# Kernel tuning notes

Measured on AMD Instinct MI355X. Metric: run time of the kernel, lower is better.

Reference implementation:

```python
import jax, jax.numpy as jnp
import numpy as np

N, E, G = 100000, 800000, 64
F_IN, H = 92, 4
D1, D2, D3 = 32, 64, 128  # per-head out dims: hidden//2, hidden, 2*hidden
HID, LAT = 64, 128
FINAL = H * D3  # 512
NEG_SLOPE = 0.2


def _p(key, shape, scale=0.05):
    return jax.random.normal(key, shape, dtype=jnp.float32) * scale


def setup_inputs() -> dict:
    key = jax.random.key(0)
    ks = jax.random.split(key, 32)
    node_feat = jax.random.normal(ks[0], (N, F_IN), dtype=jnp.float32)
    src = jax.random.randint(ks[1], (E,), 0, N)
    dst = jax.random.randint(ks[2], (E,), 0, N)
    graph_id = jnp.sort(jax.random.randint(ks[3], (N,), 0, G))
    d = {"node_feat": node_feat, "src": src, "dst": dst, "graph_id": graph_id}
    # GAT layer params (DGL GATConv: fc no bias, attn_l/attn_r [H,D], bias [H*D])
    dims = [(F_IN, D1), (H * D1, D2), (H * D2, D3)]
    i = 4
    for li, (fi, do) in enumerate(dims, 1):
        d[f"W{li}"] = _p(ks[i], (fi, H * do)); i += 1
        d[f"al{li}"] = _p(ks[i], (H, do)); i += 1
        d[f"ar{li}"] = _p(ks[i], (H, do)); i += 1
        d[f"b{li}"] = jnp.zeros((H * do,), dtype=jnp.float32)
    # gate MLP: Linear(final, hid) -> ReLU -> Linear(hid, 1)
    d["Wg1"] = _p(ks[i], (FINAL, HID)); i += 1
    d["bg1"] = jnp.zeros((HID,), dtype=jnp.float32)
    d["Wg2"] = _p(ks[i], (HID, 1)); i += 1
    d["bg2"] = jnp.zeros((1,), dtype=jnp.float32)
    d["Wmu"] = _p(ks[i], (FINAL, LAT)); i += 1
    d["bmu"] = jnp.zeros((LAT,), dtype=jnp.float32)
    d["Wlv"] = _p(ks[i], (FINAL, LAT)); i += 1
    d["blv"] = jnp.zeros((LAT,), dtype=jnp.float32)
    return d


def gat_layer(h, W, al, ar, b, src, dst, heads, d_out):
    n = h.shape[0]
    Wh = (h @ W).reshape(n, heads, d_out)                      # [N,H,D]
    el = jnp.einsum('nhd,hd->nh', Wh, al)                      # a_l . Wh
    er = jnp.einsum('nhd,hd->nh', Wh, ar)
    e = jax.nn.leaky_relu(el[src] + er[dst], NEG_SLOPE)        # [E,H]
    m = jax.ops.segment_max(e, dst, num_segments=n)
    m = jnp.where(jnp.isfinite(m), m, 0.0)                     # zero-in-degree guard
    ex = jnp.exp(e - m[dst])
    s = jax.ops.segment_sum(ex, dst, num_segments=n)
    a = ex / jnp.maximum(s[dst], 1e-9)                         # edge softmax
    msg = a[:, :, None] * Wh[src]                              # [E,H,D] (peak intermediate)
    out = jax.ops.segment_sum(msg, dst, num_segments=n)        # scatter-aggregate
    out = out + b.reshape(1, heads, d_out)
    return out.reshape(n, heads * d_out)                       # flatten(1)


def attention_pool(h, graph_id, Wg1, bg1, Wg2, bg2, num_graphs):
    gate = jax.nn.relu(h @ Wg1 + bg1) @ Wg2 + bg2              # [N,1]
    m = jax.ops.segment_max(gate, graph_id, num_segments=num_graphs)
    ex = jnp.exp(gate - m[graph_id])
    s = jax.ops.segment_sum(ex, graph_id, num_segments=num_graphs)
    a = ex / jnp.maximum(s[graph_id], 1e-9)                    # softmax over nodes per graph
    return jax.ops.segment_sum(a * h, graph_id, num_segments=num_graphs)  # [G,final]


def reference(node_feat, src, dst, graph_id,
              W1, al1, ar1, b1, W2, al2, ar2, b2, W3, al3, ar3, b3,
              Wg1, bg1, Wg2, bg2, Wmu, bmu, Wlv, blv):
    h = jax.nn.elu(gat_layer(node_feat, W1, al1, ar1, b1, src, dst, H, D1))
    h = jax.nn.elu(gat_layer(h, W2, al2, ar2, b2, src, dst, H, D2))
    h = jax.nn.elu(gat_layer(h, W3, al3, ar3, b3, src, dst, H, D3))
    g = attention_pool(h, graph_id, Wg1, bg1, Wg2, bg2, G)
    mu = g @ Wmu + bmu
    logvar = g @ Wlv + blv
    return (mu, logvar)
```

## Files before the change

kernel.cpp:

```cpp
#include <hip/hip_runtime.h>
#include <math.h>

#define NNODES 100000
#define NEDGES 800000
#define NGRAPH 64
#define NHEAD  4
#define FINALD 512
#define HIDG   64
#define LATD   128
#define K1P    96
#define NB_SCAN 98
#define PQ     16

typedef unsigned int uint;
typedef unsigned short ushort;
typedef __attribute__((ext_vector_type(8))) short bf16x8;
typedef __attribute__((ext_vector_type(4))) float f32x4;

__device__ __forceinline__ float bflo(uint u) { return __uint_as_float(u << 16); }
__device__ __forceinline__ float bfhi(uint u) { return __uint_as_float(u & 0xffff0000u); }
__device__ __forceinline__ ushort f2bf(float f) {
    uint u = __float_as_uint(f);
    return (ushort)((u + 0x7fffu + ((u >> 16) & 1u)) >> 16);
}
__device__ __forceinline__ uint pack2(float a, float b) {
    return (uint)f2bf(a) | ((uint)f2bf(b) << 16);
}
__device__ __forceinline__ void fmabf2(float w, uint v, float& a0, float& a1) {
    a0 = fmaf(w, bflo(v), a0);
    a1 = fmaf(w, bfhi(v), a1);
}

__device__ __forceinline__ void async_copy16(const ushort* gsrc, ushort* lds_base) {
    __builtin_amdgcn_global_load_lds(
        (const __attribute__((address_space(1))) uint*)gsrc,
        (__attribute__((address_space(3))) uint*)lds_base,
        16, 0, 0);
}

__global__ void init_kernel(int* __restrict__ deg, const int* __restrict__ gid,
                            int* __restrict__ gstart) {
    int i = blockIdx.x * blockDim.x + threadIdx.x;
    if (i < NNODES) deg[i] = 0;
    if (i <= NGRAPH) {
        int lo = 0, hi = NNODES;
        while (lo < hi) {
            int mid = (lo + hi) >> 1;
            if (gid[mid] < i) lo = mid + 1; else hi = mid;
        }
        gstart[i] = lo;
    }
}
__global__ void count_kernel(const int* __restrict__ dst, int* __restrict__ deg) {
    int e = blockIdx.x * blockDim.x + threadIdx.x;
    if (e < NEDGES) atomicAdd(&deg[dst[e]], 1);
}
__global__ __launch_bounds__(1024) void scan_block_kernel(const int* __restrict__ deg,
                                                          int* __restrict__ off,
                                                          int* __restrict__ bsum) {
    __shared__ int buf[1024];
    int t = threadIdx.x;
    int i = blockIdx.x * 1024 + t;
    int x = (i < NNODES) ? deg[i] : 0;
    buf[t] = x;
    __syncthreads();
    for (int s = 1; s < 1024; s <<= 1) {
        int v = (t >= s) ? buf[t - s] : 0;
        __syncthreads();
        buf[t] += v;
        __syncthreads();
    }
    if (i < NNODES) off[i] = buf[t] - x;
    if (t == 1023) bsum[blockIdx.x] = buf[1023];
}
__global__ __launch_bounds__(128) void scan_bsum_kernel(int* __restrict__ bsum) {
    __shared__ int buf[128];
    int t = threadIdx.x;
    int x = (t < NB_SCAN) ? bsum[t] : 0;
    buf[t] = x;
    __syncthreads();
    for (int s = 1; s < 128; s <<= 1) {
        int v = (t >= s) ? buf[t - s] : 0;
        __syncthreads();
        buf[t] += v;
        __syncthreads();
    }
    if (t < NB_SCAN) bsum[t] = buf[t] - x;
    if (t == 0) bsum[NB_SCAN] = buf[NB_SCAN - 1];
}
__global__ __launch_bounds__(1024) void scan_add_kernel(int* __restrict__ off,
                                                        const int* __restrict__ bsum,
                                                        int* __restrict__ cursor) {
    int i = blockIdx.x * 1024 + threadIdx.x;
    if (i < NNODES) {
        int v = off[i] + bsum[blockIdx.x];
        off[i] = v;
        cursor[i] = v;
    }
    if (i == 0) off[NNODES] = bsum[NB_SCAN];
}
__global__ void scatter_kernel(const int* __restrict__ src, const int* __restrict__ dst,
                               int* __restrict__ cursor, int* __restrict__ src_csr) {
    int e = blockIdx.x * blockDim.x + threadIdx.x;
    if (e >= NEDGES) return;
    int p = atomicAdd(&cursor[dst[e]], 1);
    src_csr[p] = src[e];
}

#define C1 (128 * K1P)
#define C2 (256 * 128)
#define C3 (512 * 256)
#define CG (64 * 512)
#define CX (NNODES * K1P)
#define CTOT (C1 + C2 + C3 + CG + CX + NNODES)
__global__ void conv_all_kernel(const float* __restrict__ W1, const float* __restrict__ W2,
                                const float* __restrict__ W3, const float* __restrict__ Wg1,
                                const float* __restrict__ nf,
                                ushort* __restrict__ Bt1, ushort* __restrict__ Bt2,
                                ushort* __restrict__ Bt3, ushort* __restrict__ Btg,
                                ushort* __restrict__ x0, float* __restrict__ gate) {
    int i = blockIdx.x * blockDim.x + threadIdx.x;
    if (i < C1) {
        int n = i / K1P, k = i - n * K1P;
        Bt1[i] = (k < 92) ? f2bf(W1[(size_t)k * 128 + n]) : (ushort)0;
        return;
    }
    i -= C1;
    if (i < C2) {
        int n = i >> 7, k = i & 127;
        Bt2[i] = f2bf(W2[(size_t)k * 256 + n]);
        return;
    }
    i -= C2;
    if (i < C3) {
        int n = i >> 8, k = i & 255;
        Bt3[i] = f2bf(W3[(size_t)k * 512 + n]);
        return;
    }
    i -= C3;
    if (i < CG) {
        int n = i >> 9, k = i & 511;
        Btg[i] = f2bf(Wg1[(size_t)k * 64 + n]);
        return;
    }
    i -= CG;
    if (i < CX) {
        int n = i / K1P, k = i - n * K1P;
        x0[i] = (k < 92) ? f2bf(nf[(size_t)n * 92 + k]) : (ushort)0;
        return;
    }
    i -= CX;
    if (i < NNODES) gate[i] = 0.f;
}

template <int BN, int MODE>
__global__ __launch_bounds__(256) void mfma_gemm(const ushort* __restrict__ A,
                                                 const ushort* __restrict__ Bt,
                                                 const float* __restrict__ bias,
                                                 ushort* __restrict__ C,
                                                 const float* __restrict__ Wg2,
                                                 float* __restrict__ gate,
                                                 int M, int K, int N) {
    constexpr int WNS = BN / 2;
    constexpr int NT = WNS / 16;
    __shared__ ushort Alds[128][32];
    __shared__ ushort Blds[BN][32];
    int tid = threadIdx.x;
    int wave = tid >> 6, lane = tid & 63;
    int wm = wave & 1, wn = wave >> 1;
    int quad = lane >> 4, l16 = lane & 15;
    int rowBase = blockIdx.y * 128;
    int colBase = blockIdx.x * BN;

    int srow = lane >> 2;
    int scol = (lane & 3) * 8;

    f32x4 acc[4][NT];
#pragma unroll
    for (int i = 0; i < 4; i++)
#pragma unroll
        for (int j = 0; j < NT; j++) acc[i][j] = (f32x4){0.f, 0.f, 0.f, 0.f};

    for (int k0 = 0; k0 < K; k0 += 32) {
#pragma unroll
        for (int c = 0; c < 2; c++) {
            int chunk = wave * 2 + c;
            int row = rowBase + chunk * 16 + srow;
            async_copy16(&A[(size_t)row * K + k0 + scol], &Alds[chunk * 16][0]);
        }
        if constexpr (BN == 128) {
#pragma unroll
            for (int c = 0; c < 2; c++) {
                int chunk = wave * 2 + c;
                int row = colBase + chunk * 16 + srow;
                async_copy16(&Bt[(size_t)row * K + k0 + scol], &Blds[chunk * 16][0]);
            }
        } else {
            int row = colBase + wave * 16 + srow;
            async_copy16(&Bt[(size_t)row * K + k0 + scol], &Blds[wave * 16][0]);
        }
        __syncthreads();
        bf16x8 af[4], bf[NT];
#pragma unroll
        for (int i = 0; i < 4; i++)
            af[i] = *(const bf16x8*)&Alds[wm * 64 + i * 16 + l16][quad * 8];
#pragma unroll
        for (int j = 0; j < NT; j++)
            bf[j] = *(const bf16x8*)&Blds[wn * WNS + j * 16 + l16][quad * 8];
#pragma unroll
        for (int i = 0; i < 4; i++)
#pragma unroll
            for (int j = 0; j < NT; j++)
                acc[i][j] = __builtin_amdgcn_mfma_f32_16x16x32_bf16(af[i], bf[j], acc[i][j], 0, 0, 0);
        __syncthreads();
    }

    if constexpr (MODE == 0) {
#pragma unroll
        for (int i = 0; i < 4; i++) {
#pragma unroll
            for (int j = 0; j < NT; j++) {
                int col = colBase + wn * WNS + j * 16 + l16;
#pragma unroll
                for (int r = 0; r < 4; r++) {
                    int row = rowBase + wm * 64 + i * 16 + quad * 4 + r;
                    if (row < M) C[(size_t)row * N + col] = f2bf(acc[i][j][r]);
                }
            }
        }
    } else {
        float bb[NT], wg[NT];
#pragma unroll
        for (int j = 0; j < NT; j++) {
            int col = colBase + wn * WNS + j * 16 + l16;
            bb[j] = bias[col];
            wg[j] = Wg2[col];
        }
#pragma unroll
        for (int i = 0; i < 4; i++) {
            float pd[4] = {0.f, 0.f, 0.f, 0.f};
#pragma unroll
            for (int j = 0; j < NT; j++) {
#pragma unroll
                for (int r = 0; r < 4; r++) {
                    float x = fmaxf(acc[i][j][r] + bb[j], 0.f);
                    pd[r] = fmaf(x, wg[j], pd[r]);
                }
            }
#pragma unroll
            for (int m = 1; m < 16; m <<= 1)
#pragma unroll
                for (int r = 0; r < 4; r++)
                    pd[r] += __shfl_xor(pd[r], m, 64);
            if (l16 == 0) {
#pragma unroll
                for (int r = 0; r < 4; r++) {
                    int row = rowBase + wm * 64 + i * 16 + quad * 4 + r;
                    if (row < M) atomicAdd(&gate[row], pd[r]);
                }
            }
        }
    }
}

template <int HD>
__global__ __launch_bounds__(256) void eler_node(const ushort* __restrict__ Wh,
                                                 const float* __restrict__ al,
                                                 const float* __restrict__ ar,
                                                 float* __restrict__ el,
                                                 float* __restrict__ er) {
    constexpr int LPN = HD / 8;
    constexpr int NPW = 64 / LPN;
    constexpr int S = (HD / NHEAD) / 8;
    int wave = threadIdx.x >> 6;
    int lane = threadIdx.x & 63;
    int sub = lane & (LPN - 1);
    int n = blockIdx.x * (4 * NPW) + wave * NPW + lane / LPN;
    int d0 = sub * 8;
    uint4 v = *(const uint4*)&Wh[(size_t)n * HD + d0];
    float w0 = bflo(v.x), w1 = bfhi(v.x), w2 = bflo(v.y), w3 = bfhi(v.y);
    float w4 = bflo(v.z), w5 = bfhi(v.z), w6 = bflo(v.w), w7 = bfhi(v.w);
    float4 a0 = *(const float4*)&al[d0];
    float4 a1 = *(const float4*)&al[d0 + 4];
    float4 b0 = *(const float4*)&ar[d0];
    float4 b1 = *(const float4*)&ar[d0 + 4];
    float sl, sr;
    sl = w0 * a0.x; sl = fmaf(w1, a0.y, sl); sl = fmaf(w2, a0.z, sl); sl = fmaf(w3, a0.w, sl);
    sl = fmaf(w4, a1.x, sl); sl = fmaf(w5, a1.y, sl); sl = fmaf(w6, a1.z, sl); sl = fmaf(w7, a1.w, sl);
    sr = w0 * b0.x; sr = fmaf(w1, b0.y, sr); sr = fmaf(w2, b0.z, sr); sr = fmaf(w3, b0.w, sr);
    sr = fmaf(w4, b1.x, sr); sr = fmaf(w5, b1.y, sr); sr = fmaf(w6, b1.z, sr); sr = fmaf(w7, b1.w, sr);
#pragma unroll
    for (int o = S / 2; o > 0; o >>= 1) {
        sl += __shfl_down(sl, o, 64);
        sr += __shfl_down(sr, o, 64);
    }
    if ((sub & (S - 1)) == 0) {
        int h = sub / S;
        el[n * 4 + h] = sl;
        er[n * 4 + h] = sr;
    }
}

__global__ void attn_node(const int* __restrict__ src_csr, const int* __restrict__ off,
                          const float4* __restrict__ el4, const float4* __restrict__ er4,
                          float4* __restrict__ aw4, float4* __restrict__ m4) {
    int n = blockIdx.x * blockDim.x + threadIdx.x;
    if (n >= NNODES) return;
    int i0 = off[n], i1 = off[n + 1];
    float4 ern = er4[n];
    float m0 = -1e30f, m1 = -1e30f, m2 = -1e30f, m3 = -1e30f;
    for (int i = i0; i < i1; i += 8) {
        int cnt = i1 - i; if (cnt > 8) cnt = 8;
        int s8[8];
#pragma unroll
        for (int j = 0; j < 8; j++)
            if (j < cnt) s8[j] = src_csr[i + j];
        float4 e8[8];
#pragma unroll
        for (int j = 0; j < 8; j++)
            if (j < cnt) e8[j] = el4[s8[j]];
#pragma unroll
        for (int j = 0; j < 8; j++) {
            if (j < cnt) {
                float4 x = e8[j];
                x.x += ern.x; x.y += ern.y; x.z += ern.z; x.w += ern.w;
                x.x = (x.x >= 0.f) ? x.x : 0.2f * x.x;
                x.y = (x.y >= 0.f) ? x.y : 0.2f * x.y;
                x.z = (x.z >= 0.f) ? x.z : 0.2f * x.z;
                x.w = (x.w >= 0.f) ? x.w : 0.2f * x.w;
                aw4[i + j] = x;
                m0 = fmaxf(m0, x.x); m1 = fmaxf(m1, x.y);
                m2 = fmaxf(m2, x.z); m3 = fmaxf(m3, x.w);
            }
        }
    }
    m4[n] = make_float4(m0, m1, m2, m3);
}

template <int HD, int DPL, int B>
__global__ __launch_bounds__(256) void gat_aggregate4(const int* __restrict__ src_csr,
                                                      const int* __restrict__ off,
                                                      const ushort* __restrict__ Wh,
                                                      const float* __restrict__ aw,
                                                      const float* __restrict__ m4,
                                                      const float* __restrict__ bias,
                                                      ushort* __restrict__ out,
                                                      int pass) {
    constexpr int LOGD = (HD == 128) ? 5 : (HD == 256) ? 6 : 7;
    const int lane = threadIdx.x & 63;
    const int wv = __builtin_amdgcn_readfirstlane((int)(threadIdx.x >> 6));
    const int n = blockIdx.x * 4 + wv;
    const int d = pass * (64 * DPL) + lane * DPL;
    const int h = d >> LOGD;
    const int i0 = __builtin_amdgcn_readfirstlane(off[n]);
    const int i1 = __builtin_amdgcn_readfirstlane(off[n + 1]);
    const float mh = m4[n * 4 + h];

    float acc[DPL];
#pragma unroll
    for (int j = 0; j < DPL; j++) acc[j] = 0.f;
    float ssum = 0.f;
    const ushort* __restrict__ col = Wh + d;

    int i = i0;
    for (; i + B <= i1; i += B) {
        int s[B];
        float w[B];
#pragma unroll
        for (int b = 0; b < B; b++) s[b] = __builtin_amdgcn_readfirstlane(src_csr[i + b]);
#pragma unroll
        for (int b = 0; b < B; b++) w[b] = expf(aw[(size_t)(i + b) * 4 + h] - mh);
        if constexpr (DPL == 8) {
            uint4 v[B];
#pragma unroll
            for (int b = 0; b < B; b++) v[b] = *(const uint4*)&col[(size_t)s[b] * HD];
#pragma unroll
            for (int b = 0; b < B; b++) {
                ssum += w[b];
                fmabf2(w[b], v[b].x, acc[0], acc[1]);
                fmabf2(w[b], v[b].y, acc[2], acc[3]);
                fmabf2(w[b], v[b].z, acc[4], acc[5]);
                fmabf2(w[b], v[b].w, acc[6], acc[7]);
            }
        } else if constexpr (DPL == 4) {
            uint2 v[B];
#pragma unroll
            for (int b = 0; b < B; b++) v[b] = *(const uint2*)&col[(size_t)s[b] * HD];
#pragma unroll
            for (int b = 0; b < B; b++) {
                ssum += w[b];
                fmabf2(w[b], v[b].x, acc[0], acc[1]);
                fmabf2(w[b], v[b].y, acc[2], acc[3]);
            }
        } else {
            uint v[B];
#pragma unroll
            for (int b = 0; b < B; b++) v[b] = *(const uint*)&col[(size_t)s[b] * HD];
#pragma unroll
            for (int b = 0; b < B; b++) {
                ssum += w[b];
                fmabf2(w[b], v[b], acc[0], acc[1]);
            }
        }
    }
    for (; i < i1; ++i) {
        const int s0 = __builtin_amdgcn_readfirstlane(src_csr[i]);
        const float w0 = expf(aw[(size_t)i * 4 + h] - mh);
        ssum += w0;
        if constexpr (DPL == 8) {
            uint4 v0 = *(const uint4*)&col[(size_t)s0 * HD];
            fmabf2(w0, v0.x, acc[0], acc[1]);
            fmabf2(w0, v0.y, acc[2], acc[3]);
            fmabf2(w0, v0.z, acc[4], acc[5]);
            fmabf2(w0, v0.w, acc[6], acc[7]);
        } else if constexpr (DPL == 4) {
            uint2 v0 = *(const uint2*)&col[(size_t)s0 * HD];
            fmabf2(w0, v0.x, acc[0], acc[1]);
            fmabf2(w0, v0.y, acc[2], acc[3]);
        } else {
            uint v0 = *(const uint*)&col[(size_t)s0 * HD];
            fmabf2(w0, v0, acc[0], acc[1]);
        }
    }

    const float inv = 1.f / fmaxf(ssum, 1e-9f);
    float x[DPL];
#pragma unroll
    for (int j = 0; j < DPL; j++) {
        float v = acc[j] * inv + bias[d + j];
        x[j] = (v > 0.f) ? v : (expf(v) - 1.f);
    }
    if constexpr (DPL == 8) {
        uint4 o;
        o.x = pack2(x[0], x[1]); o.y = pack2(x[2], x[3]);
        o.z = pack2(x[4], x[5]); o.w = pack2(x[6], x[7]);
        *(uint4*)&out[(size_t)n * HD + d] = o;
    } else if constexpr (DPL == 4) {
        uint2 o;
        o.x = pack2(x[0], x[1]); o.y = pack2(x[2], x[3]);
        *(uint2*)&out[(size_t)n * HD + d] = o;
    } else {
        *(uint*)&out[(size_t)n * HD + d] = pack2(x[0], x[1]);
    }
}

__global__ __launch_bounds__(256) void graph_softmax_kernel(const float* __restrict__ gate,
                                                            const int* __restrict__ gstart,
                                                            float* __restrict__ exn,
                                                            float* __restrict__ gsum) {
    int g = blockIdx.x, t = threadIdx.x;
    int n0 = gstart[g], n1 = gstart[g + 1];
    __shared__ float red[256];
    float m = -1e30f;
    for (int n = n0 + t; n < n1; n += 256) m = fmaxf(m, gate[n]);
    red[t] = m; __syncthreads();
    for (int s = 128; s > 0; s >>= 1) {
        if (t < s) red[t] = fmaxf(red[t], red[t + s]);
        __syncthreads();
    }
    m = red[0]; __syncthreads();
    float sum = 0.f;
    for (int n = n0 + t; n < n1; n += 256) {
        float v = expf(gate[n] - m);
        exn[n] = v;
        sum += v;
    }
    red[t] = sum; __syncthreads();
    for (int s = 128; s > 0; s >>= 1) {
        if (t < s) red[t] += red[t + s];
        __syncthreads();
    }
    if (t == 0) gsum[g] = red[0];
}

__global__ __launch_bounds__(128) void pool_partial(const ushort* __restrict__ h,
                                                    const float* __restrict__ exn,
                                                    const int* __restrict__ gstart,
                                                    float* __restrict__ partial) {
    int g = blockIdx.x, q = blockIdx.y;
    int n0 = gstart[g], n1 = gstart[g + 1];
    int len = n1 - n0;
    int chunk = (len + PQ - 1) / PQ;
    int s = n0 + q * chunk;
    int e = s + chunk; if (e > n1) e = n1;
    int d4 = threadIdx.x;
    const uint2* h2 = (const uint2*)h;
    float a0 = 0.f, a1 = 0.f, a2 = 0.f, a3 = 0.f;
    for (int n = s; n < e; n++) {
        float w = exn[n];
        uint2 v = h2[(size_t)n * 128 + d4];
        a0 = fmaf(w, bflo(v.x), a0);
        a1 = fmaf(w, bfhi(v.x), a1);
        a2 = fmaf(w, bflo(v.y), a2);
        a3 = fmaf(w, bfhi(v.y), a3);
    }
    *(float4*)&partial[((size_t)(g * PQ + q)) * FINALD + d4 * 4] = make_float4(a0, a1, a2, a3);
}

__global__ __launch_bounds__(128) void final_kernel(const float* __restrict__ partial,
                                                    const float* __restrict__ gsum,
                                                    const float* __restrict__ Wmu,
                                                    const float* __restrict__ bmu,
                                                    const float* __restrict__ Wlv,
                                                    const float* __restrict__ blv,
                                                    float* __restrict__ out) {
    int g = blockIdx.x, j = threadIdx.x;
    __shared__ float pooled[FINALD];
    const float* p = partial + (size_t)g * PQ * FINALD;
    for (int k = j; k < FINALD; k += 128) {
        float v = 0.f;
#pragma unroll
        for (int q = 0; q < PQ; q++) v += p[q * FINALD + k];
        pooled[k] = v;
    }
    __syncthreads();
    float am = 0.f, av = 0.f;
    for (int k = 0; k < FINALD; k++) {
        float pv = pooled[k];
        am = fmaf(pv, Wmu[k * LATD + j], am);
        av = fmaf(pv, Wlv[k * LATD + j], av);
    }
    float inv = 1.f / fmaxf(gsum[g], 1e-9f);
    out[g * LATD + j] = am * inv + bmu[j];
    out[NGRAPH * LATD + g * LATD + j] = av * inv + blv[j];
}

extern "C" void kernel_launch(void* const* d_in, const int* in_sizes, int n_in,
                              void* d_out, int out_size, void* d_ws, size_t ws_size,
                              hipStream_t stream) {
    (void)in_sizes; (void)n_in; (void)out_size; (void)ws_size;
    const float* node_feat = (const float*)d_in[0];
    const int* src = (const int*)d_in[1];
    const int* dst = (const int*)d_in[2];
    const int* gid = (const int*)d_in[3];
    const float* W[3]    = {(const float*)d_in[4],  (const float*)d_in[8],  (const float*)d_in[12]};
    const float* al[3]   = {(const float*)d_in[5],  (const float*)d_in[9],  (const float*)d_in[13]};
    const float* ar[3]   = {(const float*)d_in[6],  (const float*)d_in[10], (const float*)d_in[14]};
    const float* bias[3] = {(const float*)d_in[7],  (const float*)d_in[11], (const float*)d_in[15]};
    const float* Wg1 = (const float*)d_in[16];
    const float* bg1 = (const float*)d_in[17];
    const float* Wg2 = (const float*)d_in[18];
    const float* Wmu = (const float*)d_in[20];
    const float* bmu = (const float*)d_in[21];
    const float* Wlv = (const float*)d_in[22];
    const float* blv = (const float*)d_in[23];

    char* ws = (char*)d_ws;
    size_t woff = 0;
    auto carve = [&](size_t bytes) {
        void* p = ws + woff;
        woff = (woff + bytes + 255) & ~(size_t)255;
        return p;
    };
    ushort* hA      = (ushort*)carve((size_t)NNODES * 512 * 2);
    ushort* hB      = (ushort*)carve((size_t)NNODES * 512 * 2);
    float*  el      = (float*) carve((size_t)NNODES * 4 * 4);
    float*  er      = (float*) carve((size_t)NNODES * 4 * 4);
    float*  aw      = (float*) carve((size_t)NEDGES * 4 * 4);
    float*  m4      = (float*) carve((size_t)NNODES * 4 * 4);
    int*    deg     = (int*)   carve((size_t)NNODES * 4);
    int*    off     = (int*)   carve((size_t)(NNODES + 1) * 4);
    int*    cursor  = (int*)   carve((size_t)NNODES * 4);
    int*    src_csr = (int*)   carve((size_t)NEDGES * 4);
    int*    bsum    = (int*)   carve((size_t)(NB_SCAN + 1) * 4);
    float*  gate    = (float*) carve((size_t)NNODES * 4);
    float*  exn     = (float*) carve((size_t)NNODES * 4);
    int*    gstart  = (int*)   carve((size_t)(NGRAPH + 1) * 4);
    float*  partial = (float*) carve((size_t)NGRAPH * PQ * FINALD * 4);
    float*  gsum    = (float*) carve((size_t)NGRAPH * 4);
    ushort* Bt1     = (ushort*)carve((size_t)128 * K1P * 2);
    ushort* Bt2     = (ushort*)carve((size_t)256 * 128 * 2);
    ushort* Bt3     = (ushort*)carve((size_t)512 * 256 * 2);
    ushort* Btg     = (ushort*)carve((size_t)64 * 512 * 2 + 4096);
    ushort* x0      = hA;

    init_kernel<<<(NNODES + 255) / 256, 256, 0, stream>>>(deg, gid, gstart);
    count_kernel<<<(NEDGES + 255) / 256, 256, 0, stream>>>(dst, deg);
    scan_block_kernel<<<NB_SCAN, 1024, 0, stream>>>(deg, off, bsum);
    scan_bsum_kernel<<<1, 128, 0, stream>>>(bsum);
    scan_add_kernel<<<NB_SCAN, 1024, 0, stream>>>(off, bsum, cursor);
    scatter_kernel<<<(NEDGES + 255) / 256, 256, 0, stream>>>(src, dst, cursor, src_csr);
    conv_all_kernel<<<(CTOT + 255) / 256, 256, 0, stream>>>(
        W[0], W[1], W[2], Wg1, node_feat, Bt1, Bt2, Bt3, Btg, x0, gate);

    const int MB = (NNODES + 127) / 128;
    const int AGB = NNODES / 4;

    mfma_gemm<128, 0><<<dim3(1, MB), 256, 0, stream>>>(
        x0, Bt1, nullptr, hB, nullptr, nullptr, NNODES, K1P, 128);
    eler_node<128><<<NNODES / 16, 256, 0, stream>>>(hB, al[0], ar[0], el, er);
    attn_node<<<(NNODES + 255) / 256, 256, 0, stream>>>(
        src_csr, off, (const float4*)el, (const float4*)er, (float4*)aw, (float4*)m4);
    gat_aggregate4<128, 2, 8><<<AGB, 256, 0, stream>>>(
        src_csr, off, hB, aw, m4, bias[0], hA, 0);

    mfma_gemm<128, 0><<<dim3(2, MB), 256, 0, stream>>>(
        hA, Bt2, nullptr, hB, nullptr, nullptr, NNODES, 128, 256);
    eler_node<256><<<NNODES / 8, 256, 0, stream>>>(hB, al[1], ar[1], el, er);
    attn_node<<<(NNODES + 255) / 256, 256, 0, stream>>>(
        src_csr, off, (const float4*)el, (const float4*)er, (float4*)aw, (float4*)m4);
    gat_aggregate4<256, 4, 8><<<AGB, 256, 0, stream>>>(
        src_csr, off, hB, aw, m4, bias[1], hA, 0);

    mfma_gemm<128, 0><<<dim3(4, MB), 256, 0, stream>>>(
        hA, Bt3, nullptr, hB, nullptr, nullptr, NNODES, 256, 512);
    eler_node<512><<<NNODES / 4, 256, 0, stream>>>(hB, al[2], ar[2], el, er);
    attn_node<<<(NNODES + 255) / 256, 256, 0, stream>>>(
        src_csr, off, (const float4*)el, (const float4*)er, (float4*)aw, (float4*)m4);
    gat_aggregate4<512, 4, 8><<<AGB, 256, 0, stream>>>(
        src_csr, off, hB, aw, m4, bias[2], hA, 0);
    gat_aggregate4<512, 4, 8><<<AGB, 256, 0, stream>>>(
        src_csr, off, hB, aw, m4, bias[2], hA, 1);

    mfma_gemm<64, 1><<<dim3(1, MB), 256, 0, stream>>>(
        hA, Btg, bg1, nullptr, Wg2, gate, NNODES, FINALD, HIDG);
    graph_softmax_kernel<<<NGRAPH, 256, 0, stream>>>(gate, gstart, exn, gsum);
    pool_partial<<<dim3(NGRAPH, PQ), 128, 0, stream>>>(hA, exn, gstart, partial);
    final_kernel<<<NGRAPH, 128, 0, stream>>>(partial, gsum, Wmu, bmu, Wlv, blv, (float*)d_out);
}
```

Before: 774.2 us.

## Fuse edge-softmax logit and max computation into GAT aggregation kernel

Removes the separate attn_node kernel and the per-edge aw and per-node m4 buffers. Each aggregation wavefront now computes the leaky-relu logits for up to 64 incoming edges in parallel across lanes, reduces the max and sum with shuffles, stages the exp weights in LDS, and then gathers the neighbour features. This saves a kernel launch and the edge-sized write and read per layer, and parallelises the softmax over lanes. The cost is that the logit work is repeated in each aggregation launch, twice for layer 3, and nodes with more than 64 in-edges take a slower chunked path.

```diff
diff --git a/kernel.cpp b/kernel.cpp
--- a/kernel.cpp
+++ b/kernel.cpp
@@ -29,6 +29,9 @@
 __device__ __forceinline__ void fmabf2(float w, uint v, float& a0, float& a1) {
     a0 = fmaf(w, bflo(v), a0);
     a1 = fmaf(w, bfhi(v), a1);
+}
+__device__ __forceinline__ float lrelu(float x) {
+    return (x >= 0.f) ? x : 0.2f * x;
 }
 
 __device__ __forceinline__ void async_copy16(const ushort* gsrc, ushort* lds_base) {
@@ -301,52 +304,17 @@
     }
 }
 
-__global__ void attn_node(const int* __restrict__ src_csr, const int* __restrict__ off,
-                          const float4* __restrict__ el4, const float4* __restrict__ er4,
-                          float4* __restrict__ aw4, float4* __restrict__ m4) {
-    int n = blockIdx.x * blockDim.x + threadIdx.x;
-    if (n >= NNODES) return;
-    int i0 = off[n], i1 = off[n + 1];
-    float4 ern = er4[n];
-    float m0 = -1e30f, m1 = -1e30f, m2 = -1e30f, m3 = -1e30f;
-    for (int i = i0; i < i1; i += 8) {
-        int cnt = i1 - i; if (cnt > 8) cnt = 8;
-        int s8[8];
-#pragma unroll
-        for (int j = 0; j < 8; j++)
-            if (j < cnt) s8[j] = src_csr[i + j];
-        float4 e8[8];
-#pragma unroll
-        for (int j = 0; j < 8; j++)
-            if (j < cnt) e8[j] = el4[s8[j]];
-#pragma unroll
-        for (int j = 0; j < 8; j++) {
-            if (j < cnt) {
-                float4 x = e8[j];
-                x.x += ern.x; x.y += ern.y; x.z += ern.z; x.w += ern.w;
-                x.x = (x.x >= 0.f) ? x.x : 0.2f * x.x;
-                x.y = (x.y >= 0.f) ? x.y : 0.2f * x.y;
-                x.z = (x.z >= 0.f) ? x.z : 0.2f * x.z;
-                x.w = (x.w >= 0.f) ? x.w : 0.2f * x.w;
-                aw4[i + j] = x;
-                m0 = fmaxf(m0, x.x); m1 = fmaxf(m1, x.y);
-                m2 = fmaxf(m2, x.z); m3 = fmaxf(m3, x.w);
-            }
-        }
-    }
-    m4[n] = make_float4(m0, m1, m2, m3);
-}
-
 template <int HD, int DPL, int B>
-__global__ __launch_bounds__(256) void gat_aggregate4(const int* __restrict__ src_csr,
+__global__ __launch_bounds__(256) void gat_aggregate5(const int* __restrict__ src_csr,
                                                       const int* __restrict__ off,
                                                       const ushort* __restrict__ Wh,
-                                                      const float* __restrict__ aw,
-                                                      const float* __restrict__ m4,
+                                                      const float4* __restrict__ el4,
+                                                      const float4* __restrict__ er4,
                                                       const float* __restrict__ bias,
                                                       ushort* __restrict__ out,
                                                       int pass) {
     constexpr int LOGD = (HD == 128) ? 5 : (HD == 256) ? 6 : 7;
+    __shared__ float wlds[4][256];
     const int lane = threadIdx.x & 63;
     const int wv = __builtin_amdgcn_readfirstlane((int)(threadIdx.x >> 6));
     const int n = blockIdx.x * 4 + wv;
@@ -354,7 +322,39 @@
     const int h = d >> LOGD;
     const int i0 = __builtin_amdgcn_readfirstlane(off[n]);
     const int i1 = __builtin_amdgcn_readfirstlane(off[n + 1]);
-    const float mh = m4[n * 4 + h];
+    const int deg = i1 - i0;
+    float* wl = &wlds[wv][0];
+    const float4 ern = er4[n];
+
+    float x0 = -1e30f, x1 = -1e30f, x2 = -1e30f, x3 = -1e30f;
+    const bool single = (deg <= 64);
+    if (single) {
+        if (lane < deg) {
+            int s = src_csr[i0 + lane];
+            float4 ev = el4[s];
+            x0 = lrelu(ev.x + ern.x); x1 = lrelu(ev.y + ern.y);
+            x2 = lrelu(ev.z + ern.z); x3 = lrelu(ev.w + ern.w);
+        }
+    } else {
+        for (int c = i0; c < i1; c += 64) {
+            if (c + lane < i1) {
+                int s = src_csr[c + lane];
+                float4 ev = el4[s];
+                x0 = fmaxf(x0, lrelu(ev.x + ern.x));
+                x1 = fmaxf(x1, lrelu(ev.y + ern.y));
+                x2 = fmaxf(x2, lrelu(ev.z + ern.z));
+                x3 = fmaxf(x3, lrelu(ev.w + ern.w));
+            }
+        }
+    }
+    float m0 = x0, m1 = x1, m2 = x2, m3 = x3;
+#pragma unroll
+    for (int o = 32; o > 0; o >>= 1) {
+        m0 = fmaxf(m0, __shfl_xor(m0, o, 64));
+        m1 = fmaxf(m1, __shfl_xor(m1, o, 64));
+        m2 = fmaxf(m2, __shfl_xor(m2, o, 64));
+        m3 = fmaxf(m3, __shfl_xor(m3, o, 64));
+    }
 
     float acc[DPL];
 #pragma unroll
@@ -362,64 +362,89 @@
     float ssum = 0.f;
     const ushort* __restrict__ col = Wh + d;
 
-    int i = i0;
-    for (; i + B <= i1; i += B) {
-        int s[B];
-        float w[B];
-#pragma unroll
-        for (int b = 0; b < B; b++) s[b] = __builtin_amdgcn_readfirstlane(src_csr[i + b]);
-#pragma unroll
-        for (int b = 0; b < B; b++) w[b] = expf(aw[(size_t)(i + b) * 4 + h] - mh);
-        if constexpr (DPL == 8) {
-            uint4 v[B];
-#pragma unroll
-            for (int b = 0; b < B; b++) v[b] = *(const uint4*)&col[(size_t)s[b] * HD];
-#pragma unroll
-            for (int b = 0; b < B; b++) {
-                ssum += w[b];
-                fmabf2(w[b], v[b].x, acc[0], acc[1]);
-                fmabf2(w[b], v[b].y, acc[2], acc[3]);
-                fmabf2(w[b], v[b].z, acc[4], acc[5]);
-                fmabf2(w[b], v[b].w, acc[6], acc[7]);
-            }
-        } else if constexpr (DPL == 4) {
-            uint2 v[B];
-#pragma unroll
-            for (int b = 0; b < B; b++) v[b] = *(const uint2*)&col[(size_t)s[b] * HD];
-#pragma unroll
-            for (int b = 0; b < B; b++) {
-                ssum += w[b];
-                fmabf2(w[b], v[b].x, acc[0], acc[1]);
-                fmabf2(w[b], v[b].y, acc[2], acc[3]);
+    for (int c = i0; c < i1; c += 64) {
+        float w0 = 0.f, w1 = 0.f, w2 = 0.f, w3 = 0.f;
+        if (single) {
+            if (lane < deg) {
+                w0 = expf(x0 - m0); w1 = expf(x1 - m1);
+                w2 = expf(x2 - m2); w3 = expf(x3 - m3);
             }
         } else {
-            uint v[B];
-#pragma unroll
-            for (int b = 0; b < B; b++) v[b] = *(const uint*)&col[(size_t)s[b] * HD];
-#pragma unroll
-            for (int b = 0; b < B; b++) {
-                ssum += w[b];
-                fmabf2(w[b], v[b], acc[0], acc[1]);
-            }
-        }
-    }
-    for (; i < i1; ++i) {
-        const int s0 = __builtin_amdgcn_readfirstlane(src_csr[i]);
-        const float w0 = expf(aw[(size_t)i * 4 + h] - mh);
-        ssum += w0;
-        if constexpr (DPL == 8) {
-            uint4 v0 = *(const uint4*)&col[(size_t)s0 * HD];
-            fmabf2(w0, v0.x, acc[0], acc[1]);
-            fmabf2(w0, v0.y, acc[2], acc[3]);
-            fmabf2(w0, v0.z, acc[4], acc[5]);
-            fmabf2(w0, v0.w, acc[6], acc[7]);
-        } else if constexpr (DPL == 4) {
-            uint2 v0 = *(const uint2*)&col[(size_t)s0 * HD];
-            fmabf2(w0, v0.x, acc[0], acc[1]);
-            fmabf2(w0, v0.y, acc[2], acc[3]);
-        } else {
-            uint v0 = *(const uint*)&col[(size_t)s0 * HD];
-            fmabf2(w0, v0, acc[0], acc[1]);
+            if (c + lane < i1) {
+                int s = src_csr[c + lane];
+                float4 ev = el4[s];
+                w0 = expf(lrelu(ev.x + ern.x) - m0);
+                w1 = expf(lrelu(ev.y + ern.y) - m1);
+                w2 = expf(lrelu(ev.z + ern.z) - m2);
+                w3 = expf(lrelu(ev.w + ern.w) - m3);
+            }
+        }
+        *(float4*)&wl[lane * 4] = make_float4(w0, w1, w2, w3);
+        float s0 = w0, s1 = w1, s2 = w2, s3 = w3;
+#pragma unroll
+        for (int o = 32; o > 0; o >>= 1) {
+            s0 += __shfl_xor(s0, o, 64);
+            s1 += __shfl_xor(s1, o, 64);
+            s2 += __shfl_xor(s2, o, 64);
+            s3 += __shfl_xor(s3, o, 64);
+        }
+        ssum += (h & 2) ? ((h & 1) ? s3 : s2) : ((h & 1) ? s1 : s0);
+        asm volatile("s_waitcnt lgkmcnt(0)" ::: "memory");
+
+        const int cend = (c + 64 < i1) ? (c + 64) : i1;
+        int i = c;
+        for (; i + B <= cend; i += B) {
+            int s[B];
+            float w[B];
+#pragma unroll
+            for (int b = 0; b < B; b++) s[b] = __builtin_amdgcn_readfirstlane(src_csr[i + b]);
+#pragma unroll
+            for (int b = 0; b < B; b++) w[b] = wl[(i - c + b) * 4 + h];
+            if constexpr (DPL == 8) {
+                uint4 v[B];
+#pragma unroll
+                for (int b = 0; b < B; b++) v[b] = *(const uint4*)&col[(size_t)s[b] * HD];
+#pragma unroll
+                for (int b = 0; b < B; b++) {
+                    fmabf2(w[b], v[b].x, acc[0], acc[1]);
+                    fmabf2(w[b], v[b].y, acc[2], acc[3]);
+                    fmabf2(w[b], v[b].z, acc[4], acc[5]);
+                    fmabf2(w[b], v[b].w, acc[6], acc[7]);
+                }
+            } else if constexpr (DPL == 4) {
+                uint2 v[B];
+#pragma unroll
+                for (int b = 0; b < B; b++) v[b] = *(const uint2*)&col[(size_t)s[b] * HD];
+#pragma unroll
+                for (int b = 0; b < B; b++) {
+                    fmabf2(w[b], v[b].x, acc[0], acc[1]);
+                    fmabf2(w[b], v[b].y, acc[2], acc[3]);
+                }
+            } else {
+                uint v[B];
+#pragma unroll
+                for (int b = 0; b < B; b++) v[b] = *(const uint*)&col[(size_t)s[b] * HD];
+#pragma unroll
+                for (int b = 0; b < B; b++) fmabf2(w[b], v[b], acc[0], acc[1]);
+            }
+        }
+        for (; i < cend; ++i) {
+            const int s0i = __builtin_amdgcn_readfirstlane(src_csr[i]);
+            const float w0i = wl[(i - c) * 4 + h];
+            if constexpr (DPL == 8) {
+                uint4 v0 = *(const uint4*)&col[(size_t)s0i * HD];
+                fmabf2(w0i, v0.x, acc[0], acc[1]);
+                fmabf2(w0i, v0.y, acc[2], acc[3]);
+                fmabf2(w0i, v0.z, acc[4], acc[5]);
+                fmabf2(w0i, v0.w, acc[6], acc[7]);
+            } else if constexpr (DPL == 4) {
+                uint2 v0 = *(const uint2*)&col[(size_t)s0i * HD];
+                fmabf2(w0i, v0.x, acc[0], acc[1]);
+                fmabf2(w0i, v0.y, acc[2], acc[3]);
+            } else {
+                uint v0 = *(const uint*)&col[(size_t)s0i * HD];
+                fmabf2(w0i, v0, acc[0], acc[1]);
+            }
         }
     }
 
@@ -556,8 +581,6 @@
     ushort* hB      = (ushort*)carve((size_t)NNODES * 512 * 2);
     float*  el      = (float*) carve((size_t)NNODES * 4 * 4);
     float*  er      = (float*) carve((size_t)NNODES * 4 * 4);
-    float*  aw      = (float*) carve((size_t)NEDGES * 4 * 4);
-    float*  m4      = (float*) carve((size_t)NNODES * 4 * 4);
     int*    deg     = (int*)   carve((size_t)NNODES * 4);
     int*    off     = (int*)   carve((size_t)(NNODES + 1) * 4);
     int*    cursor  = (int*)   carve((size_t)NNODES * 4);
@@ -589,28 +612,22 @@
     mfma_gemm<128, 0><<<dim3(1, MB), 256, 0, stream>>>(
         x0, Bt1, nullptr, hB, nullptr, nullptr, NNODES, K1P, 128);
     eler_node<128><<<NNODES / 16, 256, 0, stream>>>(hB, al[0], ar[0], el, er);
-    attn_node<<<(NNODES + 255) / 256, 256, 0, stream>>>(
-        src_csr, off, (const float4*)el, (const float4*)er, (float4*)aw, (float4*)m4);
-    gat_aggregate4<128, 2, 8><<<AGB, 256, 0, stream>>>(
-        src_csr, off, hB, aw, m4, bias[0], hA, 0);
+    gat_aggregate5<128, 2, 8><<<AGB, 256, 0, stream>>>(
+        src_csr, off, hB, (const float4*)el, (const float4*)er, bias[0], hA, 0);
 
     mfma_gemm<128, 0><<<dim3(2, MB), 256, 0, stream>>>(
         hA, Bt2, nullptr, hB, nullptr, nullptr, NNODES, 128, 256);
     eler_node<256><<<NNODES / 8, 256, 0, stream>>>(hB, al[1], ar[1], el, er);
-    attn_node<<<(NNODES + 255) / 256, 256, 0, stream>>>(
-        src_csr, off, (const float4*)el, (const float4*)er, (float4*)aw, (float4*)m4);
-    gat_aggregate4<256, 4, 8><<<AGB, 256, 0, stream>>>(
-        src_csr, off, hB, aw, m4, bias[1], hA, 0);
+    gat_aggregate5<256, 4, 8><<<AGB, 256, 0, stream>>>(
+        src_csr, off, hB, (const float4*)el, (const float4*)er, bias[1], hA, 0);
 
     mfma_gemm<128, 0><<<dim3(4, MB), 256, 0, stream>>>(
         hA, Bt3, nullptr, hB, nullptr, nullptr, NNODES, 256, 512);
     eler_node<512><<<NNODES / 4, 256, 0, stream>>>(hB, al[2], ar[2], el, er);
-    attn_node<<<(NNODES + 255) / 256, 256, 0, stream>>>(
-        src_csr, off, (const float4*)el, (const float4*)er, (float4*)aw, (float4*)m4);
-    gat_aggregate4<512, 4, 8><<<AGB, 256, 0, stream>>>(
-        src_csr, off, hB, aw, m4, bias[2], hA, 0);
-    gat_aggregate4<512, 4, 8><<<AGB, 256, 0, stream>>>(
-        src_csr, off, hB, aw, m4, bias[2], hA, 1);
+    gat_aggregate5<512, 4, 8><<<AGB, 256, 0, stream>>>(
+        src_csr, off, hB, (const float4*)el, (const float4*)er, bias[2], hA, 0);
+    gat_aggregate5<512, 4, 8><<<AGB, 256, 0, stream>>>(
+        src_csr, off, hB, (const float4*)el, (const float4*)er, bias[2], hA, 1);
 
     mfma_gemm<64, 1><<<dim3(1, MB), 256, 0, stream>>>(
         hA, Btg, bg1, nullptr, Wg2, gate, NNODES, FINALD, HIDG);
```

Result: slower. 854.5 us (+10.4%).
